# Kernel optimization log

Hardware: AMD Instinct MI355X
Metric: run time of the kernel (lower is better)

## Reference

```python
import jax, jax.numpy as jnp
import numpy as np

B, L, IDIM = 2, 4096, 2048
N_HEADS, N_GROUPS, HEAD_DIM = 16, 4, 128
GROUP_SIZE = N_HEADS // N_GROUPS
WINDOW = 1024
SCALE = 256.0 ** -0.5  # query_pre_attn_scalar = 256
EPS = 1e-6


def setup_inputs() -> dict:
    key = jax.random.key(0)
    ks = jax.random.split(key, 8)
    x = jax.random.normal(ks[0], (B, L, IDIM), dtype=jnp.float32)
    # realistic RoPE tables
    inv_freq = 1.0 / (10000.0 ** (np.arange(0, HEAD_DIM, 2, dtype=np.float32) / HEAD_DIM))
    t = np.arange(L, dtype=np.float32)
    freqs = np.outer(t, inv_freq)                      # [L, HEAD_DIM//2]
    emb = np.concatenate([freqs, freqs], axis=-1)      # [L, HEAD_DIM]
    cos = jnp.asarray(np.cos(emb), dtype=jnp.float32)
    sin = jnp.asarray(np.sin(emb), dtype=jnp.float32)
    s = 0.02
    Wq = jax.random.normal(ks[1], (IDIM, N_HEADS * HEAD_DIM), dtype=jnp.float32) * s
    Wk = jax.random.normal(ks[2], (IDIM, N_GROUPS * HEAD_DIM), dtype=jnp.float32) * s
    Wv = jax.random.normal(ks[3], (IDIM, N_GROUPS * HEAD_DIM), dtype=jnp.float32) * s
    Wo = jax.random.normal(ks[4], (N_HEADS * HEAD_DIM, IDIM), dtype=jnp.float32) * s
    qn_w = jnp.ones((HEAD_DIM,), dtype=jnp.float32)
    kn_w = jnp.ones((HEAD_DIM,), dtype=jnp.float32)
    return {"x": x, "cos": cos, "sin": sin, "Wq": Wq, "Wk": Wk, "Wv": Wv, "Wo": Wo, "qn_w": qn_w, "kn_w": kn_w}


def _rmsnorm(x, w):
    var = jnp.mean(jnp.square(x), axis=-1, keepdims=True)
    return x * jax.lax.rsqrt(var + EPS) * w


def _rope(x, cos, sin):
    # x: [b, h, l, d]; cos/sin: [l, d]
    d2 = x.shape[-1] // 2
    x1, x2 = x[..., :d2], x[..., d2:]
    rot = jnp.concatenate([-x2, x1], axis=-1)
    return x * cos[None, None] + rot * sin[None, None]


def reference(x, cos, sin, Wq, Wk, Wv, Wo, qn_w, kn_w):
    b, l, _ = x.shape
    q = (x @ Wq).reshape(b, l, N_HEADS, HEAD_DIM).transpose(0, 2, 1, 3)   # b h l d
    k = (x @ Wk).reshape(b, l, N_GROUPS, HEAD_DIM).transpose(0, 2, 1, 3)  # b g l d
    v = (x @ Wv).reshape(b, l, N_GROUPS, HEAD_DIM).transpose(0, 2, 1, 3)  # b g l d
    q = _rmsnorm(q, qn_w)
    k = _rmsnorm(k, kn_w)
    q = _rope(q, cos, sin)
    k = _rope(k, cos, sin)
    k = jnp.repeat(k, GROUP_SIZE, axis=1)  # b h l d
    v = jnp.repeat(v, GROUP_SIZE, axis=1)
    dots = jnp.einsum('bhid,bhjd->bhij', q, k) * SCALE
    i = jnp.arange(l)[:, None]
    j = jnp.arange(l)[None, :]
    allowed = (j <= i) & (j > i - WINDOW)  # causal sliding window
    dots = jnp.where(allowed[None, None], dots, -jnp.inf)
    attn = jax.nn.softmax(dots, axis=-1)
    out = jnp.einsum('bhij,bhjd->bhid', attn, v)
    out = out.transpose(0, 2, 1, 3).reshape(b, l, N_HEADS * HEAD_DIM)
    return out @ Wo
```

## Files before the change

kernel.cpp:

```cpp
#include <hip/hip_runtime.h>
#include <hip/hip_bf16.h>

typedef __hip_bfloat16 bf16;
typedef __attribute__((ext_vector_type(8))) __bf16 bf16x8;
typedef __attribute__((ext_vector_type(4))) float f32x4;

#define MFMA16(a, b, c) __builtin_amdgcn_mfma_f32_16x16x32_bf16((a), (b), (c), 0, 0, 0)

static __device__ __forceinline__ void gload_lds16(const void* g, void* l) {
    typedef const __attribute__((address_space(1))) unsigned gq_t;
    typedef __attribute__((address_space(3))) unsigned ls_t;
    __builtin_amdgcn_global_load_lds((gq_t*)g, (ls_t*)l, 16, 0, 0);
}

static __device__ __forceinline__ unsigned short f2bfbits(float f) {
    bf16 h = __float2bfloat16(f);
    return *reinterpret_cast<unsigned short*>(&h);
}

__global__ __launch_bounds__(256) void cvt_bf16_kernel(const float* __restrict__ in,
                                                       bf16* __restrict__ out, int n) {
    int i = (blockIdx.x * 256 + threadIdx.x) * 8;
    if (i < n) {
        float4 a = *reinterpret_cast<const float4*>(in + i);
        float4 b = *reinterpret_cast<const float4*>(in + i + 4);
        bf16 tmp[8];
        tmp[0] = __float2bfloat16(a.x); tmp[1] = __float2bfloat16(a.y);
        tmp[2] = __float2bfloat16(a.z); tmp[3] = __float2bfloat16(a.w);
        tmp[4] = __float2bfloat16(b.x); tmp[5] = __float2bfloat16(b.y);
        tmp[6] = __float2bfloat16(b.z); tmp[7] = __float2bfloat16(b.w);
        *reinterpret_cast<uint4*>(out + i) = *reinterpret_cast<const uint4*>(tmp);
    }
}

__global__ __launch_bounds__(256) void transpose_wqkv_kernel(const float* __restrict__ Wq,
                                                             const float* __restrict__ Wk,
                                                             const float* __restrict__ Wv,
                                                             bf16* __restrict__ out) {
    __shared__ float tile[32][33];
    int k0 = blockIdx.x * 32;
    int n0 = blockIdx.y * 32;
    int tx = threadIdx.x & 31, ty = threadIdx.x >> 5;
#pragma unroll
    for (int i = 0; i < 4; ++i) {
        int k = k0 + ty + i * 8, n = n0 + tx;
        float v;
        if (n < 2048)      v = Wq[(size_t)k * 2048 + n];
        else if (n < 2560) v = Wk[(size_t)k * 512 + (n - 2048)];
        else               v = Wv[(size_t)k * 512 + (n - 2560)];
        tile[ty + i * 8][tx] = v;
    }
    __syncthreads();
#pragma unroll
    for (int i = 0; i < 4; ++i)
        out[(size_t)(n0 + ty + i * 8) * 2048 + k0 + tx] = __float2bfloat16(tile[tx][ty + i * 8]);
}

__global__ __launch_bounds__(256) void transpose_w_kernel(const float* __restrict__ in,
                                                          bf16* __restrict__ out) {
    __shared__ float tile[32][33];
    int k0 = blockIdx.x * 32, n0 = blockIdx.y * 32;
    int tx = threadIdx.x & 31, ty = threadIdx.x >> 5;
#pragma unroll
    for (int i = 0; i < 4; ++i)
        tile[ty + i * 8][tx] = in[(size_t)(k0 + ty + i * 8) * 2048 + n0 + tx];
    __syncthreads();
#pragma unroll
    for (int i = 0; i < 4; ++i)
        out[(size_t)(n0 + ty + i * 8) * 2048 + k0 + tx] = __float2bfloat16(tile[tx][ty + i * 8]);
}

template <int NFRAG, bool OUT_F32>
__global__ __launch_bounds__(512, 2) void gemm8p_kernel(const bf16* __restrict__ A,
                                                        const bf16* __restrict__ BT,
                                                        void* __restrict__ Cv,
                                                        int M, int N, int K, int nbn) {
    constexpr int BN = NFRAG * 64;
    constexpr int PB = NFRAG;
    __shared__ bf16 As[2][256 * 64];
    __shared__ bf16 Bs[2][BN * 64];
    int t = threadIdx.x;
    int lane = t & 63, w = t >> 6;
    int wm = w >> 2, wn = w & 3;
    int lr = lane & 15, lq = lane >> 4;
    int lin = blockIdx.x;
    int cpx = gridDim.x >> 3;
    int wg = (lin & 7) * cpx + (lin >> 3);
    int bm = wg / nbn, bn = wg % nbn;
    const bf16* Ab = A + (size_t)bm * 256 * K;
    const bf16* Bb = BT + (size_t)bn * BN * K;

    auto stA = [&](int slot, int kt, int piece) {
        int idx = piece * 512 + t;
        int r = idx >> 3, c8 = idx & 7;
        gload_lds16(Ab + (size_t)r * K + kt * 64 + ((c8 ^ (r & 7)) * 8), &As[slot][idx * 8]);
    };
    auto stB = [&](int slot, int kt, int piece) {
        int idx = piece * 512 + t;
        int r = idx >> 3, c8 = idx & 7;
        gload_lds16(Bb + (size_t)r * K + kt * 64 + ((c8 ^ (r & 7)) * 8), &Bs[slot][idx * 8]);
    };

    f32x4 acc[8][NFRAG] = {};
    bf16x8 bq[NFRAG][2], af[2][2];

    auto readB = [&](int slot) {
#pragma unroll
        for (int n = 0; n < NFRAG; ++n)
#pragma unroll
            for (int ks = 0; ks < 2; ++ks) {
                int ro = wn * (NFRAG * 16) + n * 16 + lr;
                int ch = (ks * 4 + lq) ^ (ro & 7);
                bq[n][ks] = *reinterpret_cast<const bf16x8*>(&Bs[slot][ro * 64 + ch * 8]);
            }
    };
    auto readA = [&](int mbase, int slot) {
#pragma unroll
        for (int mi = 0; mi < 2; ++mi)
#pragma unroll
            for (int ks = 0; ks < 2; ++ks) {
                int ro = wm * 128 + (mbase + mi) * 16 + lr;
                int ch = (ks * 4 + lq) ^ (ro & 7);
                af[mi][ks] = *reinterpret_cast<const bf16x8*>(&As[slot][ro * 64 + ch * 8]);
            }
    };
    auto mf = [&](int mbase) {
#pragma unroll
        for (int mi = 0; mi < 2; ++mi)
#pragma unroll
            for (int n = 0; n < NFRAG; ++n)
#pragma unroll
                for (int ks = 0; ks < 2; ++ks)
                    acc[mbase + mi][n] = MFMA16(af[mi][ks], bq[n][ks], acc[mbase + mi][n]);
    };

#define GATE_PB()                                                          \
    do {                                                                   \
        if constexpr (NFRAG == 4) asm volatile("s_waitcnt vmcnt(4)" ::: "memory"); \
        else                      asm volatile("s_waitcnt vmcnt(3)" ::: "memory"); \
    } while (0)
#define PHASE_TAIL()                                                       \
    do {                                                                   \
        __builtin_amdgcn_s_barrier();                                      \
        asm volatile("s_waitcnt lgkmcnt(0)" ::: "memory");                 \
    } while (0)
#define MFMA_CLUSTER(mb)                                                   \
    do {                                                                   \
        __builtin_amdgcn_s_setprio(1);                                     \
        mf(mb);                                                            \
        __builtin_amdgcn_s_setprio(0);                                     \
        __builtin_amdgcn_s_barrier();                                      \
    } while (0)

    int nkt = K >> 6;
#pragma unroll
    for (int p = 0; p < 4; ++p) stA(0, 0, p);
#pragma unroll
    for (int p = 0; p < PB; ++p) stB(0, 0, p);
#pragma unroll
    for (int p = 0; p < PB; ++p) stB(1, 1, p);
    GATE_PB();
    __builtin_amdgcn_s_barrier();

    int nI = nkt >> 1;
    for (int I = 0; I < nI; ++I) {
        int T = I << 1;
        bool s2 = (T + 2) < nkt, s3 = (T + 3) < nkt;
        readB(0); readA(0, 0);
#pragma unroll
        for (int p = 0; p < 4; ++p) stA(1, T + 1, p);
        PHASE_TAIL();
        MFMA_CLUSTER(0);
        readA(2, 0);
        if (s2) { stB(0, T + 2, 0); stB(0, T + 2, 1); }
        PHASE_TAIL();
        MFMA_CLUSTER(2);
        readA(4, 0);
        if (s2) {
#pragma unroll
            for (int p = 2; p < PB; ++p) stB(0, T + 2, p);
        }
        PHASE_TAIL();
        MFMA_CLUSTER(4);
        readA(6, 0);
        if (s2) GATE_PB();
        else    asm volatile("s_waitcnt vmcnt(0)" ::: "memory");
        PHASE_TAIL();
        MFMA_CLUSTER(6);
        readB(1); readA(0, 1);
        if (s2) {
#pragma unroll
            for (int p = 0; p < 4; ++p) stA(0, T + 2, p);
        }
        PHASE_TAIL();
        MFMA_CLUSTER(0);
        readA(2, 1);
        if (s3) { stB(1, T + 3, 0); stB(1, T + 3, 1); }
        PHASE_TAIL();
        MFMA_CLUSTER(2);
        readA(4, 1);
        if (s3) {
#pragma unroll
            for (int p = 2; p < PB; ++p) stB(1, T + 3, p);
        }
        PHASE_TAIL();
        MFMA_CLUSTER(4);
        readA(6, 1);
        if (s3) GATE_PB();
        else    asm volatile("s_waitcnt vmcnt(0)" ::: "memory");
        PHASE_TAIL();
        MFMA_CLUSTER(6);
    }
#undef GATE_PB
#undef PHASE_TAIL
#undef MFMA_CLUSTER

#pragma unroll
    for (int m = 0; m < 8; ++m)
#pragma unroll
        for (int n = 0; n < NFRAG; ++n) {
            int row = bm * 256 + wm * 128 + m * 16 + lq * 4;
            int col = bn * BN + wn * (NFRAG * 16) + n * 16 + lr;
#pragma unroll
            for (int j = 0; j < 4; ++j) {
                if (OUT_F32)
                    ((float*)Cv)[(size_t)(row + j) * N + col] = acc[m][n][j];
                else
                    ((bf16*)Cv)[(size_t)(row + j) * N + col] = __float2bfloat16(acc[m][n][j]);
            }
        }
}

__global__ __launch_bounds__(256) void normrope_kernel(const bf16* __restrict__ qkv,
                                                       const float* __restrict__ cosT,
                                                       const float* __restrict__ sinT,
                                                       const float* __restrict__ qnw,
                                                       const float* __restrict__ knw,
                                                       bf16* __restrict__ qh,
                                                       bf16* __restrict__ kh) {
    int t = threadIdx.x;
    int lane = t & 63, wv = t >> 6;
    int blk = blockIdx.x;
    int r = blk / 5;
    int s = (blk % 5) * 4 + wv;
    int b = r >> 12, l = r & 4095;
    int e0 = lane * 2;
    const bf16* src = qkv + (size_t)r * 3072 + s * 128;
    ushort2 xu = *reinterpret_cast<const ushort2*>(src + e0);
    float v0 = __uint_as_float((unsigned)xu.x << 16);
    float v1 = __uint_as_float((unsigned)xu.y << 16);
    float ss = v0 * v0 + v1 * v1;
#pragma unroll
    for (int d = 1; d < 64; d <<= 1) ss += __shfl_xor(ss, d, 64);
    float rn = rsqrtf(ss * (1.0f / 128.0f) + 1e-6f);
    const float* wn = (s < 16) ? qnw : knw;
    float2 wv2 = *reinterpret_cast<const float2*>(wn + e0);
    float xn0 = v0 * rn * wv2.x;
    float xn1 = v1 * rn * wv2.y;
    float xp0 = __shfl_xor(xn0, 32, 64);
    float xp1 = __shfl_xor(xn1, 32, 64);
    float r0 = (lane < 32) ? -xp0 : xp0;
    float r1 = (lane < 32) ? -xp1 : xp1;
    float2 c2 = *reinterpret_cast<const float2*>(cosT + (size_t)l * 128 + e0);
    float2 s2 = *reinterpret_cast<const float2*>(sinT + (size_t)l * 128 + e0);
    float o0 = xn0 * c2.x + r0 * s2.x;
    float o1 = xn1 * c2.y + r1 * s2.y;
    ushort2 ou;
    if (s < 16) {
        const float scl = 0.0625f * 1.44269504088896f;
        ou.x = f2bfbits(o0 * scl);
        ou.y = f2bfbits(o1 * scl);
        bf16* dst = qh + ((size_t)(b * 16 + s) * 4096 + l) * 128;
        *reinterpret_cast<ushort2*>(dst + e0) = ou;
    } else {
        int g = s - 16;
        ou.x = f2bfbits(o0);
        ou.y = f2bfbits(o1);
        int sw = (l & 7) << 3;
        bf16* dst = kh + ((size_t)(b * 4 + g) * 4096 + l) * 128;
        *reinterpret_cast<ushort2*>(dst + (e0 ^ sw)) = ou;
    }
}

__global__ __launch_bounds__(256) void vtrans_kernel(const bf16* __restrict__ qkv,
                                                     bf16* __restrict__ vt) {
    __shared__ bf16 tile[64][132];
    int t = threadIdx.x;
    int l0 = blockIdx.x * 64;
    int bg = blockIdx.y;
    int b = bg >> 2, g = bg & 3;
    const bf16* src = qkv + ((size_t)(b * 4096 + l0)) * 3072 + 2560 + g * 128;
#pragma unroll
    for (int i = 0; i < 4; ++i) {
        int c = i * 256 + t;
        int r = c >> 4, c16 = c & 15;
        uint4 v = *reinterpret_cast<const uint4*>(src + (size_t)r * 3072 + c16 * 8);
        *reinterpret_cast<uint2*>(&tile[r][c16 * 8]) = make_uint2(v.x, v.y);
        *reinterpret_cast<uint2*>(&tile[r][c16 * 8 + 4]) = make_uint2(v.z, v.w);
    }
    __syncthreads();
    bf16* dst = vt + (size_t)bg * 128 * 4096 + l0;
    int cj = t & 63;
    int pos = (cj & 0x23) | ((cj & 16) >> 2) | ((cj & 12) << 1);
#pragma unroll
    for (int dd = 0; dd < 32; ++dd) {
        int d = (t >> 6) * 32 + dd;
        dst[(size_t)d * 4096 + (pos ^ ((d & 7) << 3))] = tile[cj][d];
    }
}

__global__ __launch_bounds__(512, 2) void attn_kernel(const bf16* __restrict__ qh,
                                                      const bf16* __restrict__ kh,
                                                      const bf16* __restrict__ vt,
                                                      bf16* __restrict__ ao) {
    __shared__ bf16 Ks[2][64 * 128];
    __shared__ bf16 Vs[2][128 * 64];
    int t = threadIdx.x;
    int lane = t & 63, w = t >> 6;
    int lr = lane & 15, lq = lane >> 4;
    int bid = blockIdx.x;
    int bh = (bid & 7) * 4 + (bid >> 7);
    int qs = ((bid >> 3) & 15) * 256;
    int b = bh >> 4, h = bh & 15, g = h >> 2;
    int row0 = qs + w * 32;
    const bf16* qp = qh + ((size_t)(b * 16 + h) * 4096 + row0) * 128;
    const bf16* kp = kh + (size_t)(b * 4 + g) * 4096 * 128;
    const bf16* vp = vt + (size_t)(b * 4 + g) * 128 * 4096;

    bf16x8 aq[2][4];
#pragma unroll
    for (int g2 = 0; g2 < 2; ++g2)
#pragma unroll
        for (int kk = 0; kk < 4; ++kk)
            aq[g2][kk] = *reinterpret_cast<const bf16x8*>(qp + (size_t)(g2 * 16 + lr) * 128 + kk * 32 + lq * 8);

    f32x4 o0[8] = {}, o1[8] = {};
    float lsum0 = 0.f, lsum1 = 0.f;
    int qi0 = row0 + lr, qi1 = row0 + 16 + lr;
    int sA = max(0, row0 - 1023) >> 6;
    int sB = max(0, row0 + 16 - 1023) >> 6;
    int t1w = row0 >> 6;
    int t0w = sA;
    int t0 = max(0, qs - 1023) >> 6;
    int t1 = (qs + 255) >> 6;

    auto stage = [&](int buf, int kt) {
        int j0 = kt * 64;
        const bf16* kg = kp + (size_t)j0 * 128;
#pragma unroll
        for (int i = 0; i < 2; ++i) {
            int c = i * 512 + t;
            gload_lds16(kg + c * 8, &Ks[buf][c * 8]);
        }
#pragma unroll
        for (int i = 0; i < 2; ++i) {
            int c = i * 512 + t;
            int d = c >> 3, co = (c & 7) * 8;
            gload_lds16(vp + (size_t)d * 4096 + j0 + co, &Vs[buf][c * 8]);
        }
    };

    stage(0, t0);
    int cur = 0;

    for (int kt = t0; kt <= t1; ++kt) {
        if (kt < t1) {
            stage(cur ^ 1, kt + 1);
            asm volatile("s_waitcnt vmcnt(4)" ::: "memory");
        } else {
            asm volatile("s_waitcnt vmcnt(0)" ::: "memory");
        }
        __builtin_amdgcn_s_barrier();
        if (kt >= t0w && kt <= t1w) {
            int j0 = kt * 64;
            f32x4 s0[4] = {}, s1[4] = {};
            __builtin_amdgcn_s_setprio(1);
#pragma unroll
            for (int jt = 0; jt < 4; ++jt) {
                int r = jt * 16 + lr;
                int rs = (r & 7) << 3;
#pragma unroll
                for (int kk = 0; kk < 4; ++kk) {
                    int c = kk * 32 + lq * 8;
                    bf16x8 bk = *reinterpret_cast<const bf16x8*>(&Ks[cur][r * 128 + (c ^ rs)]);
                    s0[jt] = MFMA16(bk, aq[0][kk], s0[jt]);
                    s1[jt] = MFMA16(bk, aq[1][kk], s1[jt]);
                }
            }
            __builtin_amdgcn_s_setprio(0);
            if (kt <= sA + 1 || kt == t1w) {
#pragma unroll
                for (int jt = 0; jt < 4; ++jt)
#pragma unroll
                    for (int j = 0; j < 4; ++j) {
                        int kj = j0 + jt * 16 + lq * 4 + j;
                        if (!(kj <= qi0 && kj > qi0 - 1024)) s0[jt][j] = -1e30f;
                    }
            }
            if (kt <= sB + 1 || kt == t1w) {
#pragma unroll
                for (int jt = 0; jt < 4; ++jt)
#pragma unroll
                    for (int j = 0; j < 4; ++j) {
                        int kj = j0 + jt * 16 + lq * 4 + j;
                        if (!(kj <= qi1 && kj > qi1 - 1024)) s1[jt][j] = -1e30f;
                    }
            }
            unsigned pk0[4][2], pk1[4][2];
#pragma unroll
            for (int jt = 0; jt < 4; ++jt)
#pragma unroll
                for (int hh = 0; hh < 2; ++hh) {
                    float p0 = exp2f(s0[jt][2 * hh] - 11.5415603f);
                    float p1 = exp2f(s0[jt][2 * hh + 1] - 11.5415603f);
                    lsum0 += p0 + p1;
                    asm("v_cvt_pk_bf16_f32 %0, %1, %2" : "=v"(pk0[jt][hh]) : "v"(p0), "v"(p1));
                }
#pragma unroll
            for (int jt = 0; jt < 4; ++jt)
#pragma unroll
                for (int hh = 0; hh < 2; ++hh) {
                    float p0 = exp2f(s1[jt][2 * hh] - 11.5415603f);
                    float p1 = exp2f(s1[jt][2 * hh + 1] - 11.5415603f);
                    lsum1 += p0 + p1;
                    asm("v_cvt_pk_bf16_f32 %0, %1, %2" : "=v"(pk1[jt][hh]) : "v"(p0), "v"(p1));
                }
            __builtin_amdgcn_s_setprio(1);
#pragma unroll
            for (int kk2 = 0; kk2 < 2; ++kk2) {
                union { unsigned u[4]; bf16x8 v; } pu0, pu1;
                pu0.u[0] = pk0[2 * kk2][0]; pu0.u[1] = pk0[2 * kk2][1];
                pu0.u[2] = pk0[2 * kk2 + 1][0]; pu0.u[3] = pk0[2 * kk2 + 1][1];
                pu1.u[0] = pk1[2 * kk2][0]; pu1.u[1] = pk1[2 * kk2][1];
                pu1.u[2] = pk1[2 * kk2 + 1][0]; pu1.u[3] = pk1[2 * kk2 + 1][1];
#pragma unroll
                for (int dt = 0; dt < 8; ++dt) {
                    int r = dt * 16 + lr;
                    int c = kk2 * 32 + lq * 8;
                    bf16x8 bv = *reinterpret_cast<const bf16x8*>(&Vs[cur][r * 64 + (c ^ ((r & 7) << 3))]);
                    o0[dt] = MFMA16(pu0.v, bv, o0[dt]);
                    o1[dt] = MFMA16(pu1.v, bv, o1[dt]);
                }
            }
            __builtin_amdgcn_s_setprio(0);
        }
        __builtin_amdgcn_s_barrier();
        cur ^= 1;
    }
    float lt0 = lsum0, lt1 = lsum1;
    lt0 += __shfl_xor(lt0, 16, 64);  lt0 += __shfl_xor(lt0, 32, 64);
    lt1 += __shfl_xor(lt1, 16, 64);  lt1 += __shfl_xor(lt1, 32, 64);
    float li0 = 1.0f / lt0, li1 = 1.0f / lt1;
    float lv0[4], lv1[4];
#pragma unroll
    for (int j = 0; j < 4; ++j) {
        lv0[j] = __shfl(li0, lq * 4 + j, 64);
        lv1[j] = __shfl(li1, lq * 4 + j, 64);
    }
#pragma unroll
    for (int dt = 0; dt < 8; ++dt)
#pragma unroll
        for (int j = 0; j < 4; ++j) {
            size_t base = (size_t)(b * 4096 + row0 + lq * 4 + j) * 2048 + h * 128 + dt * 16 + lr;
            ao[base] = __float2bfloat16(o0[dt][j] * lv0[j]);
            ao[base + (size_t)16 * 2048] = __float2bfloat16(o1[dt][j] * lv1[j]);
        }
}

extern "C" void kernel_launch(void* const* d_in, const int* in_sizes, int n_in,
                              void* d_out, int out_size, void* d_ws, size_t ws_size,
                              hipStream_t stream) {
    const float* x    = (const float*)d_in[0];
    const float* cosT = (const float*)d_in[1];
    const float* sinT = (const float*)d_in[2];
    const float* Wq   = (const float*)d_in[3];
    const float* Wk   = (const float*)d_in[4];
    const float* Wv   = (const float*)d_in[5];
    const float* Wo   = (const float*)d_in[6];
    const float* qnw  = (const float*)d_in[7];
    const float* knw  = (const float*)d_in[8];

    char* ws = (char*)d_ws;
    bf16* xb    = (bf16*)(ws);
    bf16* wqkvT = (bf16*)(ws + 33554432);
    bf16* woT   = (bf16*)(ws + 46137344);
    bf16* qh    = (bf16*)(ws + 54525952);
    bf16* kh    = (bf16*)(ws + 88080384);
    bf16* vt    = (bf16*)(ws + 96468992);
    bf16* ao    = xb;
    bf16* qkv   = (bf16*)d_out;

    cvt_bf16_kernel<<<8192, 256, 0, stream>>>(x, xb, 16777216);
    transpose_wqkv_kernel<<<dim3(64, 96), 256, 0, stream>>>(Wq, Wk, Wv, wqkvT);
    transpose_w_kernel<<<dim3(64, 64), 256, 0, stream>>>(Wo, woT);
    gemm8p_kernel<4, false><<<384, 512, 0, stream>>>(xb, wqkvT, (void*)qkv, 8192, 3072, 2048, 12);
    normrope_kernel<<<40960, 256, 0, stream>>>(qkv, cosT, sinT, qnw, knw, qh, kh);
    vtrans_kernel<<<dim3(64, 8), 256, 0, stream>>>(qkv, vt);
    attn_kernel<<<512, 512, 0, stream>>>(qh, kh, vt, ao);
    gemm8p_kernel<4, true><<<256, 512, 0, stream>>>(ao, woT, d_out, 8192, 2048, 2048, 8);
}
```

Baseline: 366.6 us.

## Double-buffer LDS fragment reads in GEMM and retile QKV projection to NFRAG=3

The GEMM main loop now double-buffers its A and B register fragments. The next phase's LDS reads are issued before the current MFMA cluster, and the explicit lgkmcnt(0) wait after each barrier is removed, so LDS latency overlaps with matrix math. The QKV projection GEMM also switches to NFRAG=3 with 512 workgroups instead of 384, giving a narrower N tile and more blocks to fill the CUs. The cost is higher register pressure from the duplicated fragments. The vmcnt gate is now tied to PB, and correctness depends on the compiler inserting the right LDS waits.

```diff
diff --git a/kernel.cpp b/kernel.cpp
--- a/kernel.cpp
+++ b/kernel.cpp
@@ -102,29 +102,29 @@
     };
 
     f32x4 acc[8][NFRAG] = {};
-    bf16x8 bq[NFRAG][2], af[2][2];
-
-    auto readB = [&](int slot) {
+    bf16x8 bqA[NFRAG][2], bqB[NFRAG][2], afA[2][2], afB[2][2];
+
+    auto issueB = [&](bf16x8 (&dst)[NFRAG][2], int slot) {
 #pragma unroll
         for (int n = 0; n < NFRAG; ++n)
 #pragma unroll
             for (int ks = 0; ks < 2; ++ks) {
                 int ro = wn * (NFRAG * 16) + n * 16 + lr;
                 int ch = (ks * 4 + lq) ^ (ro & 7);
-                bq[n][ks] = *reinterpret_cast<const bf16x8*>(&Bs[slot][ro * 64 + ch * 8]);
-            }
-    };
-    auto readA = [&](int mbase, int slot) {
+                dst[n][ks] = *reinterpret_cast<const bf16x8*>(&Bs[slot][ro * 64 + ch * 8]);
+            }
+    };
+    auto issueA = [&](bf16x8 (&dst)[2][2], int mbase, int slot) {
 #pragma unroll
         for (int mi = 0; mi < 2; ++mi)
 #pragma unroll
             for (int ks = 0; ks < 2; ++ks) {
                 int ro = wm * 128 + (mbase + mi) * 16 + lr;
                 int ch = (ks * 4 + lq) ^ (ro & 7);
-                af[mi][ks] = *reinterpret_cast<const bf16x8*>(&As[slot][ro * 64 + ch * 8]);
-            }
-    };
-    auto mf = [&](int mbase) {
+                dst[mi][ks] = *reinterpret_cast<const bf16x8*>(&As[slot][ro * 64 + ch * 8]);
+            }
+    };
+    auto mf = [&](bf16x8 (&af)[2][2], bf16x8 (&bq)[NFRAG][2], int mbase) {
 #pragma unroll
         for (int mi = 0; mi < 2; ++mi)
 #pragma unroll
@@ -134,20 +134,11 @@
                     acc[mbase + mi][n] = MFMA16(af[mi][ks], bq[n][ks], acc[mbase + mi][n]);
     };
 
-#define GATE_PB()                                                          \
-    do {                                                                   \
-        if constexpr (NFRAG == 4) asm volatile("s_waitcnt vmcnt(4)" ::: "memory"); \
-        else                      asm volatile("s_waitcnt vmcnt(3)" ::: "memory"); \
-    } while (0)
-#define PHASE_TAIL()                                                       \
-    do {                                                                   \
-        __builtin_amdgcn_s_barrier();                                      \
-        asm volatile("s_waitcnt lgkmcnt(0)" ::: "memory");                 \
-    } while (0)
-#define MFMA_CLUSTER(mb)                                                   \
+#define GATE_PB() asm volatile("s_waitcnt vmcnt(%0)" :: "i"(PB) : "memory")
+#define MFMA_CLUSTER(af, bq, mb)                                           \
     do {                                                                   \
         __builtin_amdgcn_s_setprio(1);                                     \
-        mf(mb);                                                            \
+        mf(af, bq, mb);                                                    \
         __builtin_amdgcn_s_setprio(0);                                     \
         __builtin_amdgcn_s_barrier();                                      \
     } while (0)
@@ -161,58 +152,58 @@
     for (int p = 0; p < PB; ++p) stB(1, 1, p);
     GATE_PB();
     __builtin_amdgcn_s_barrier();
+    issueB(bqA, 0); issueA(afA, 0, 0);
 
     int nI = nkt >> 1;
     for (int I = 0; I < nI; ++I) {
         int T = I << 1;
         bool s2 = (T + 2) < nkt, s3 = (T + 3) < nkt;
-        readB(0); readA(0, 0);
 #pragma unroll
         for (int p = 0; p < 4; ++p) stA(1, T + 1, p);
-        PHASE_TAIL();
-        MFMA_CLUSTER(0);
-        readA(2, 0);
+        __builtin_amdgcn_s_barrier();
+        issueA(afB, 2, 0);
+        MFMA_CLUSTER(afA, bqA, 0);
         if (s2) { stB(0, T + 2, 0); stB(0, T + 2, 1); }
-        PHASE_TAIL();
-        MFMA_CLUSTER(2);
-        readA(4, 0);
+        __builtin_amdgcn_s_barrier();
+        issueA(afA, 4, 0);
+        MFMA_CLUSTER(afB, bqA, 2);
         if (s2) {
 #pragma unroll
             for (int p = 2; p < PB; ++p) stB(0, T + 2, p);
         }
-        PHASE_TAIL();
-        MFMA_CLUSTER(4);
-        readA(6, 0);
+        __builtin_amdgcn_s_barrier();
+        issueA(afB, 6, 0);
+        MFMA_CLUSTER(afA, bqA, 4);
         if (s2) GATE_PB();
         else    asm volatile("s_waitcnt vmcnt(0)" ::: "memory");
-        PHASE_TAIL();
-        MFMA_CLUSTER(6);
-        readB(1); readA(0, 1);
+        __builtin_amdgcn_s_barrier();
+        issueB(bqB, 1); issueA(afA, 0, 1);
+        MFMA_CLUSTER(afB, bqA, 6);
         if (s2) {
 #pragma unroll
             for (int p = 0; p < 4; ++p) stA(0, T + 2, p);
         }
-        PHASE_TAIL();
-        MFMA_CLUSTER(0);
-        readA(2, 1);
+        __builtin_amdgcn_s_barrier();
+        issueA(afB, 2, 1);
+        MFMA_CLUSTER(afA, bqB, 0);
         if (s3) { stB(1, T + 3, 0); stB(1, T + 3, 1); }
-        PHASE_TAIL();
-        MFMA_CLUSTER(2);
-        readA(4, 1);
+        __builtin_amdgcn_s_barrier();
+        issueA(afA, 4, 1);
+        MFMA_CLUSTER(afB, bqB, 2);
         if (s3) {
 #pragma unroll
             for (int p = 2; p < PB; ++p) stB(1, T + 3, p);
         }
-        PHASE_TAIL();
-        MFMA_CLUSTER(4);
-        readA(6, 1);
+        __builtin_amdgcn_s_barrier();
+        issueA(afB, 6, 1);
+        MFMA_CLUSTER(afA, bqB, 4);
         if (s3) GATE_PB();
         else    asm volatile("s_waitcnt vmcnt(0)" ::: "memory");
-        PHASE_TAIL();
-        MFMA_CLUSTER(6);
+        __builtin_amdgcn_s_barrier();
+        if (I + 1 < nI) { issueB(bqA, 0); issueA(afA, 0, 0); }
+        MFMA_CLUSTER(afB, bqB, 6);
     }
 #undef GATE_PB
-#undef PHASE_TAIL
 #undef MFMA_CLUSTER
 
 #pragma unroll
@@ -493,7 +484,7 @@
     cvt_bf16_kernel<<<8192, 256, 0, stream>>>(x, xb, 16777216);
     transpose_wqkv_kernel<<<dim3(64, 96), 256, 0, stream>>>(Wq, Wk, Wv, wqkvT);
     transpose_w_kernel<<<dim3(64, 64), 256, 0, stream>>>(Wo, woT);
-    gemm8p_kernel<4, false><<<384, 512, 0, stream>>>(xb, wqkvT, (void*)qkv, 8192, 3072, 2048, 12);
+    gemm8p_kernel<3, false><<<512, 512, 0, stream>>>(xb, wqkvT, (void*)qkv, 8192, 3072, 2048, 16);
     normrope_kernel<<<40960, 256, 0, stream>>>(qkv, cosT, sinT, qnw, knw, qh, kh);
     vtrans_kernel<<<dim3(64, 8), 256, 0, stream>>>(qkv, vt);
     attn_kernel<<<512, 512, 0, stream>>>(qh, kh, vt, ao);
```

New measurement: 401.5 us. 9.5% more time.
